# Performance work log

Hardware: AMD Instinct MI355X
Metric: run time of the kernel (lower is better)

Reference implementation:

```python
import jax, jax.numpy as jnp
import numpy as np

B, HH, WW = 4, 192, 192
DIM, HEADS, WIN, SHIFT, HID = 256, 8, 8, 4, 1024
EPS = 1e-5


def _rel_index(w):
    coords = np.stack(np.meshgrid(np.arange(w), np.arange(w), indexing='ij')).reshape(2, -1)
    rel = coords[:, :, None] - coords[:, None, :]            # [2, N, N]
    rel = rel.transpose(1, 2, 0).astype(np.int64)
    rel[:, :, 0] += w - 1
    rel[:, :, 1] += w - 1
    rel[:, :, 0] *= 2 * w - 1
    return rel.sum(-1)                                        # [N, N]


def _ln(x, g, b):
    m = x.mean(-1, keepdims=True)
    v = ((x - m) ** 2).mean(-1, keepdims=True)
    return (x - m) / jnp.sqrt(v + EPS) * g + b


def setup_inputs() -> dict:
    key = jax.random.key(0)
    ks = jax.random.split(key, 8)
    s = 0.02
    return {
        'x': jax.random.normal(ks[0], (B, HH * WW, DIM), jnp.float32),
        'norm1_g': jnp.ones((DIM,), jnp.float32),
        'norm1_b': jnp.zeros((DIM,), jnp.float32),
        'qkv_w': s * jax.random.normal(ks[1], (DIM, 3 * DIM), jnp.float32),
        'qkv_b': jnp.zeros((3 * DIM,), jnp.float32),
        'bias_table': s * jax.random.normal(ks[2], ((2 * WIN - 1) ** 2, HEADS), jnp.float32),
        'proj_w': s * jax.random.normal(ks[3], (DIM, DIM), jnp.float32),
        'proj_b': jnp.zeros((DIM,), jnp.float32),
        'norm2_g': jnp.ones((DIM,), jnp.float32),
        'norm2_b': jnp.zeros((DIM,), jnp.float32),
        'fc1_w': s * jax.random.normal(ks[4], (DIM, HID), jnp.float32),
        'fc1_b': jnp.zeros((HID,), jnp.float32),
        'fc2_w': s * jax.random.normal(ks[5], (HID, DIM), jnp.float32),
        'fc2_b': jnp.zeros((DIM,), jnp.float32),
        'H': HH,
        'W': WW,
    }


def reference(x, norm1_g, norm1_b, qkv_w, qkv_b, bias_table, proj_w, proj_b,
              norm2_g, norm2_b, fc1_w, fc1_b, fc2_w, fc2_b, H, W):
    Bn, L, C = x.shape
    hd = C // HEADS
    win = min(WIN, H, W)
    shift = SHIFT if win > SHIFT else 0
    shortcut = x

    h = _ln(x, norm1_g, norm1_b).reshape(Bn, H, W, C)
    pad_b = (win - H % win) % win
    pad_r = (win - W % win) % win
    h = jnp.pad(h, ((0, 0), (0, pad_b), (0, pad_r), (0, 0)))
    Hp, Wp = H + pad_b, W + pad_r
    if shift > 0:
        h = jnp.roll(h, (-shift, -shift), axis=(1, 2))

    nh, nw = Hp // win, Wp // win
    h = h.reshape(Bn, nh, win, nw, win, C).transpose(0, 1, 3, 2, 4, 5)
    h = h.reshape(Bn * nh * nw, win * win, C)
    N = win * win

    # windowed attention
    qkv = (h @ qkv_w + qkv_b).reshape(-1, N, 3, HEADS, hd)
    q, k, v = qkv[:, :, 0], qkv[:, :, 1], qkv[:, :, 2]      # [Bw, N, H, hd]
    scale = hd ** -0.5
    attn = jnp.einsum('bqhd,bkhd->bhqk', q * scale, k)
    rel_idx = jnp.asarray(_rel_index(win))                   # [N, N]
    bias = bias_table[rel_idx.reshape(-1)].reshape(N, N, HEADS).transpose(2, 0, 1)
    attn = jax.nn.softmax(attn + bias[None], axis=-1)
    o = jnp.einsum('bhqk,bkhd->bqhd', attn, v).reshape(-1, N, C)
    o = o @ proj_w + proj_b

    # window reverse
    o = o.reshape(Bn, nh, nw, win, win, C).transpose(0, 1, 3, 2, 4, 5).reshape(Bn, Hp, Wp, C)
    if shift > 0:
        o = jnp.roll(o, (shift, shift), axis=(1, 2))
    o = o[:, :H, :W, :].reshape(Bn, H * W, C)

    x = shortcut + o
    m = _ln(x, norm2_g, norm2_b)
    m = jax.nn.gelu(m @ fc1_w + fc1_b, approximate=False) @ fc2_w + fc2_b
    return x + m
```

## Files before the change

### kernel.cpp

```cpp
#include <hip/hip_runtime.h>


#define SHIFT_ 4

typedef __attribute__((ext_vector_type(8))) short short8;
typedef __attribute__((ext_vector_type(4))) float floatx4;

__device__ __forceinline__ unsigned short f2b(float f) {
  union { float f; unsigned int i; } c; c.f = f;
  unsigned int u = c.i;
  return (unsigned short)((u + 0x7FFFu + ((u >> 16) & 1u)) >> 16);
}

__device__ __forceinline__ float fast_gelu(float v) {
  const float u = v * v;
  const float z = v * (2.3022082f + 0.10294326f * u);
  const float e = __builtin_amdgcn_exp2f(z);
  const float r = __builtin_amdgcn_rcpf(1.f + e);
  return v - v * r;
}

__device__ __forceinline__ void load_lds16(const void* g, void* l) {
  __builtin_amdgcn_global_load_lds((__attribute__((address_space(1))) void*)g,
                                   (__attribute__((address_space(3))) void*)l, 16, 0, 0);
}

__device__ __forceinline__ size_t tok_of_row(int row) {
  int widx = row >> 6, t = row & 63;
  int b = widx / 576; int rem = widx - b * 576;
  int wy = rem / 24, wx = rem - wy * 24;
  int ti = t >> 3, tj = t & 7;
  int gr = wy * 8 + ti + SHIFT_; if (gr >= 192) gr -= 192;
  int gc = wx * 8 + tj + SHIFT_; if (gc >= 192) gc -= 192;
  return (size_t)b * 36864 + (size_t)(gr * 192 + gc);
}

template<int SHUFFLE>
__global__ __launch_bounds__(256) void ln_kernel(const float* __restrict__ src,
    const float* __restrict__ gw, const float* __restrict__ bw,
    unsigned short* __restrict__ dst) {
  const int lane = threadIdx.x & 63;
  const int m = blockIdx.x * 4 + (threadIdx.x >> 6);
  const size_t soff = SHUFFLE ? tok_of_row(m) * 256 : (size_t)m * 256;
  float4 xv = *(const float4*)(src + soff + lane * 4);
  float s  = xv.x + xv.y + xv.z + xv.w;
  float s2 = xv.x * xv.x + xv.y * xv.y + xv.z * xv.z + xv.w * xv.w;
  #pragma unroll
  for (int off = 32; off > 0; off >>= 1) { s += __shfl_xor(s, off); s2 += __shfl_xor(s2, off); }
  const float mean = s * 0.00390625f;
  const float var  = s2 * 0.00390625f - mean * mean;
  const float rstd = rsqrtf(var + 1e-5f);
  float4 gv = *(const float4*)(gw + lane * 4);
  float4 bv = *(const float4*)(bw + lane * 4);
  ushort4 o;
  o.x = f2b((xv.x - mean) * rstd * gv.x + bv.x);
  o.y = f2b((xv.y - mean) * rstd * gv.y + bv.y);
  o.z = f2b((xv.z - mean) * rstd * gv.z + bv.z);
  o.w = f2b((xv.w - mean) * rstd * gv.w + bv.w);
  *(ushort4*)(dst + (size_t)m * 256 + lane * 4) = o;
}

__global__ void wconv(const float* __restrict__ W, unsigned short* __restrict__ Wt,
                      int K, int N) {
  const int idx = blockIdx.x * 256 + threadIdx.x;
  const int n = idx / K, k = idx - n * K;
  Wt[idx] = f2b(W[(size_t)k * N + n]);
}

template<int MODE>
__global__ __launch_bounds__(256) void gemm_bt(
    const unsigned short* __restrict__ A, const unsigned short* __restrict__ Wt,
    const float* __restrict__ bias, const float* __restrict__ X,
    unsigned short* __restrict__ outb, float* __restrict__ outf,
    int Ntot, int K) {
  __shared__ unsigned short sm[16384];
  const int tid = threadIdx.x;
  const int wave = tid >> 6, lane = tid & 63;
  const int lr = lane & 15, lg = lane >> 4;
  const int wm = wave >> 1, wn = wave & 1;
  const int m0 = blockIdx.y * 128, n0 = blockIdx.x * 128;

  const unsigned short* rbase = (wave < 2) ? (A + (size_t)m0 * K)
                                           : (Wt + (size_t)n0 * K);
  unsigned short* ldsbase = &sm[wave * 4096];
  const int rc0 = (wave & 1) * 8;
  int off[8];
  #pragma unroll
  for (int t = 0; t < 8; ++t) {
    const int P = (rc0 + t) * 64 + lane;
    const int r = P >> 3, c = (P & 7) ^ (r & 7);
    off[t] = r * K + c * 8;
  }

  floatx4 acc[4][4];
  #pragma unroll
  for (int i = 0; i < 4; ++i)
    #pragma unroll
    for (int j = 0; j < 4; ++j) acc[i][j] = (floatx4)0.f;

  for (int k0 = 0; k0 < K; k0 += 64) {
    __syncthreads();
    #pragma unroll
    for (int t = 0; t < 8; ++t)
      load_lds16(rbase + (off[t] + k0), ldsbase + t * 512);
    __syncthreads();
    #pragma unroll
    for (int kk = 0; kk < 2; ++kk) {
      short8 af[4], bf[4];
      #pragma unroll
      for (int mi = 0; mi < 4; ++mi) {
        const int r = wm * 64 + mi * 16 + lr;
        af[mi] = *(const short8*)&sm[r * 64 + (((kk * 4 + lg) ^ (r & 7)) * 8)];
      }
      #pragma unroll
      for (int ni = 0; ni < 4; ++ni) {
        const int r = wn * 64 + ni * 16 + lr;
        bf[ni] = *(const short8*)&sm[8192 + r * 64 + (((kk * 4 + lg) ^ (r & 7)) * 8)];
      }
      #pragma unroll
      for (int mi = 0; mi < 4; ++mi)
        #pragma unroll
        for (int ni = 0; ni < 4; ++ni)
          acc[mi][ni] = __builtin_amdgcn_mfma_f32_16x16x32_bf16(af[mi], bf[ni], acc[mi][ni], 0, 0, 0);
    }
  }

  #pragma unroll
  for (int mi = 0; mi < 4; ++mi) {
    #pragma unroll
    for (int r = 0; r < 4; ++r) {
      const int row = m0 + wm * 64 + mi * 16 + lg * 4 + r;
      size_t obase;
      if (MODE == 1) obase = tok_of_row(row) * 256;
      else obase = (size_t)row * Ntot;
      #pragma unroll
      for (int ni = 0; ni < 4; ++ni) {
        const int col = n0 + wn * 64 + ni * 16 + lr;
        const float v = acc[mi][ni][r] + bias[col];
        if (MODE == 0) {
          outb[obase + col] = f2b(v);
        } else {
          outf[obase + col] = X[obase + col] + v;
        }
      }
    }
  }
}

__global__ __launch_bounds__(256, 2) void mlp_fused(
    float* xio, const float* __restrict__ gw, const float* __restrict__ bw,
    const unsigned short* __restrict__ w1, const float* __restrict__ b1,
    const unsigned short* __restrict__ w2, const float* __restrict__ b2) {
  __shared__ unsigned short smA[16384];
  __shared__ unsigned short smH[16384];
  const int tid = threadIdx.x;
  const int wave = tid >> 6, lane = tid & 63;
  const int lr = lane & 15, lg = lane >> 4;
  const int m0 = blockIdx.x * 64;

  {
    const float4 gv = *(const float4*)(gw + lane * 4);
    const float4 bv = *(const float4*)(bw + lane * 4);
    for (int rr = 0; rr < 16; ++rr) {
      const int row = wave * 16 + rr;
      float4 xv = *(const float4*)(xio + (size_t)(m0 + row) * 256 + lane * 4);
      float s  = xv.x + xv.y + xv.z + xv.w;
      float s2 = xv.x * xv.x + xv.y * xv.y + xv.z * xv.z + xv.w * xv.w;
      #pragma unroll
      for (int off = 32; off > 0; off >>= 1) { s += __shfl_xor(s, off); s2 += __shfl_xor(s2, off); }
      const float mean = s * 0.00390625f;
      const float var  = s2 * 0.00390625f - mean * mean;
      const float rstd = rsqrtf(var + 1e-5f);
      ushort4 o;
      o.x = f2b((xv.x - mean) * rstd * gv.x + bv.x);
      o.y = f2b((xv.y - mean) * rstd * gv.y + bv.y);
      o.z = f2b((xv.z - mean) * rstd * gv.z + bv.z);
      o.w = f2b((xv.w - mean) * rstd * gv.w + bv.w);
      const int idx = row * 256 + ((((lane >> 1) ^ (row & 7))) << 3) + (lane & 1) * 4;
      *(ushort4*)&smA[idx] = o;
    }
  }
  __syncthreads();

  float b2v[4];
  #pragma unroll
  for (int ni = 0; ni < 4; ++ni) b2v[ni] = b2[wave * 64 + ni * 16 + lr];

  floatx4 acc2[4][4];
  #pragma unroll
  for (int i = 0; i < 4; ++i)
    #pragma unroll
    for (int j = 0; j < 4; ++j) acc2[i][j] = (floatx4)0.f;

  for (int q = 0; q < 4; ++q) {
    floatx4 acc1[4][4];
    #pragma unroll
    for (int i = 0; i < 4; ++i)
      #pragma unroll
      for (int j = 0; j < 4; ++j) acc1[i][j] = (floatx4)0.f;

    const unsigned short* w1q = w1 + (size_t)(q * 256 + wave * 64) * 256;
    #pragma unroll
    for (int kk = 0; kk < 8; ++kk) {
      short8 af[4], bf[4];
      #pragma unroll
      for (int mi = 0; mi < 4; ++mi) {
        const int r = mi * 16 + lr;
        af[mi] = *(const short8*)&smA[r * 256 + (((kk * 4 + lg) ^ (r & 7)) << 3)];
      }
      #pragma unroll
      for (int ni = 0; ni < 4; ++ni)
        bf[ni] = *(const short8*)(w1q + (ni * 16 + lr) * 256 + kk * 32 + lg * 8);
      #pragma unroll
      for (int mi = 0; mi < 4; ++mi)
        #pragma unroll
        for (int ni = 0; ni < 4; ++ni)
          acc1[mi][ni] = __builtin_amdgcn_mfma_f32_16x16x32_bf16(af[mi], bf[ni], acc1[mi][ni], 0, 0, 0);
    }

    float b1v[4];
    #pragma unroll
    for (int ni = 0; ni < 4; ++ni) b1v[ni] = b1[q * 256 + wave * 64 + ni * 16 + lr];

    __syncthreads();
    #pragma unroll
    for (int mi = 0; mi < 4; ++mi)
      #pragma unroll
      for (int r = 0; r < 4; ++r) {
        const int row = mi * 16 + lg * 4 + r;
        const int rbase = row * 256, rx = row & 7;
        #pragma unroll
        for (int ni = 0; ni < 4; ++ni) {
          const int col = wave * 64 + ni * 16 + lr;
          const float v = acc1[mi][ni][r] + b1v[ni];
          smH[rbase + (((col >> 3) ^ rx) << 3) + (lr & 7)] = f2b(fast_gelu(v));
        }
      }
    __syncthreads();

    const unsigned short* w2q = w2 + q * 256;
    #pragma unroll
    for (int kk = 0; kk < 8; ++kk) {
      short8 af[4], bf[4];
      #pragma unroll
      for (int mi = 0; mi < 4; ++mi) {
        const int r = mi * 16 + lr;
        af[mi] = *(const short8*)&smH[r * 256 + (((kk * 4 + lg) ^ (r & 7)) << 3)];
      }
      #pragma unroll
      for (int ni = 0; ni < 4; ++ni)
        bf[ni] = *(const short8*)(w2q + (size_t)(wave * 64 + ni * 16 + lr) * 1024 + kk * 32 + lg * 8);
      #pragma unroll
      for (int mi = 0; mi < 4; ++mi)
        #pragma unroll
        for (int ni = 0; ni < 4; ++ni)
          acc2[mi][ni] = __builtin_amdgcn_mfma_f32_16x16x32_bf16(af[mi], bf[ni], acc2[mi][ni], 0, 0, 0);
    }
  }

  #pragma unroll
  for (int mi = 0; mi < 4; ++mi)
    #pragma unroll
    for (int r = 0; r < 4; ++r) {
      const size_t gbase = (size_t)(m0 + mi * 16 + lg * 4 + r) * 256;
      #pragma unroll
      for (int ni = 0; ni < 4; ++ni) {
        const int col = wave * 64 + ni * 16 + lr;
        xio[gbase + col] += acc2[mi][ni][r] + b2v[ni];
      }
    }
}

__global__ __launch_bounds__(64) void attn_kernel(const unsigned short* __restrict__ qkv,
    const float* __restrict__ btab, unsigned short* __restrict__ obuf) {
  __shared__ unsigned short vts[2048];
  __shared__ unsigned short ps[4096];
  __shared__ float bs[225];
  const int l = threadIdx.x;
  const int win = blockIdx.x >> 3, head = blockIdx.x & 7;
  const int lr = l & 15, lg = l >> 4;
  const unsigned short* base = qkv + (size_t)(win * 64) * 768 + head * 32;

  #pragma unroll
  for (int c = 0; c < 8; ++c) {
    ushort4 vv = *(const ushort4*)(base + (size_t)l * 768 + 512 + c * 4);
    #pragma unroll
    for (int j = 0; j < 4; ++j) {
      const int d = c * 4 + j;
      const unsigned short val = j == 0 ? vv.x : j == 1 ? vv.y : j == 2 ? vv.z : vv.w;
      vts[d * 64 + (((l >> 3) ^ (d & 7)) * 8) + (l & 7)] = val;
    }
  }
  for (int i = l; i < 225; i += 64) bs[i] = btab[i * 8 + head];

  short8 af[4], bfr[4];
  #pragma unroll
  for (int mi = 0; mi < 4; ++mi)
    af[mi] = *(const short8*)(base + (size_t)(mi * 16 + lr) * 768 + lg * 8);
  #pragma unroll
  for (int ni = 0; ni < 4; ++ni)
    bfr[ni] = *(const short8*)(base + (size_t)(ni * 16 + lr) * 768 + 256 + lg * 8);

  floatx4 sa[4][4];
  #pragma unroll
  for (int mi = 0; mi < 4; ++mi)
    #pragma unroll
    for (int ni = 0; ni < 4; ++ni)
      sa[mi][ni] = __builtin_amdgcn_mfma_f32_16x16x32_bf16(af[mi], bfr[ni], (floatx4)0.f, 0, 0, 0);

  __syncthreads();

  const float scale = 0.17677669529663687f;
  #pragma unroll
  for (int mi = 0; mi < 4; ++mi) {
    #pragma unroll
    for (int r = 0; r < 4; ++r) {
      const int qi = mi * 16 + lg * 4 + r;
      const int ti = qi >> 3, tj = qi & 7;
      float vals[4];
      #pragma unroll
      for (int ni = 0; ni < 4; ++ni) {
        const int kc = ni * 16 + lr;
        const int tk = kc >> 3, tl = kc & 7;
        vals[ni] = sa[mi][ni][r] * scale + bs[(ti - tk + 7) * 15 + (tj - tl + 7)];
      }
      float mx = fmaxf(fmaxf(vals[0], vals[1]), fmaxf(vals[2], vals[3]));
      #pragma unroll
      for (int off = 1; off < 16; off <<= 1) mx = fmaxf(mx, __shfl_xor(mx, off, 16));
      float se = 0.f;
      #pragma unroll
      for (int ni = 0; ni < 4; ++ni) { vals[ni] = __expf(vals[ni] - mx); se += vals[ni]; }
      #pragma unroll
      for (int off = 1; off < 16; off <<= 1) se += __shfl_xor(se, off, 16);
      const float inv = 1.f / se;
      #pragma unroll
      for (int ni = 0; ni < 4; ++ni) {
        const int col = ni * 16 + lr;
        const int cell = col >> 3;
        ps[qi * 64 + ((cell ^ (qi & 7)) * 8) + (col & 7)] = f2b(vals[ni] * inv);
      }
    }
  }
  __syncthreads();

  floatx4 oa[4][2];
  #pragma unroll
  for (int mi = 0; mi < 4; ++mi) { oa[mi][0] = (floatx4)0.f; oa[mi][1] = (floatx4)0.f; }
  #pragma unroll
  for (int kk = 0; kk < 2; ++kk) {
    short8 pa[4], vb[2];
    #pragma unroll
    for (int mi = 0; mi < 4; ++mi) {
      const int r = mi * 16 + lr;
      pa[mi] = *(const short8*)&ps[r * 64 + (((kk * 4 + lg) ^ (r & 7)) * 8)];
    }
    #pragma unroll
    for (int nj = 0; nj < 2; ++nj) {
      const int r = nj * 16 + lr;
      vb[nj] = *(const short8*)&vts[r * 64 + (((kk * 4 + lg) ^ (r & 7)) * 8)];
    }
    #pragma unroll
    for (int mi = 0; mi < 4; ++mi)
      #pragma unroll
      for (int nj = 0; nj < 2; ++nj)
        oa[mi][nj] = __builtin_amdgcn_mfma_f32_16x16x32_bf16(pa[mi], vb[nj], oa[mi][nj], 0, 0, 0);
  }
  #pragma unroll
  for (int mi = 0; mi < 4; ++mi)
    #pragma unroll
    for (int nj = 0; nj < 2; ++nj)
      #pragma unroll
      for (int r = 0; r < 4; ++r) {
        const int row = mi * 16 + lg * 4 + r, d = nj * 16 + lr;
        obuf[(size_t)(win * 64 + row) * 256 + head * 32 + d] = f2b(oa[mi][nj][r]);
      }
}

extern "C" void kernel_launch(void* const* d_in, const int* in_sizes, int n_in,
                              void* d_out, int out_size, void* d_ws, size_t ws_size,
                              hipStream_t stream) {
  (void)in_sizes; (void)n_in; (void)out_size; (void)ws_size;
  const float* x      = (const float*)d_in[0];
  const float* n1g    = (const float*)d_in[1];
  const float* n1b    = (const float*)d_in[2];
  const float* qkv_w  = (const float*)d_in[3];
  const float* qkv_b  = (const float*)d_in[4];
  const float* btab   = (const float*)d_in[5];
  const float* proj_w = (const float*)d_in[6];
  const float* proj_b = (const float*)d_in[7];
  const float* n2g    = (const float*)d_in[8];
  const float* n2b    = (const float*)d_in[9];
  const float* fc1_w  = (const float*)d_in[10];
  const float* fc1_b  = (const float*)d_in[11];
  const float* fc2_w  = (const float*)d_in[12];
  const float* fc2_b  = (const float*)d_in[13];
  float* out = (float*)d_out;

  char* wsb = (char*)d_ws;
  unsigned short* wqkv  = (unsigned short*)(wsb);
  unsigned short* wproj = (unsigned short*)(wsb + 393216);
  unsigned short* wfc1  = (unsigned short*)(wsb + 524288);
  unsigned short* wfc2  = (unsigned short*)(wsb + 1048576);
  unsigned short* hbuf  = (unsigned short*)(wsb + 1572864);
  unsigned short* big   = (unsigned short*)(wsb + 77070336);

  wconv<<<768, 256, 0, stream>>>(qkv_w, wqkv, 256, 768);
  wconv<<<256, 256, 0, stream>>>(proj_w, wproj, 256, 256);
  wconv<<<1024, 256, 0, stream>>>(fc1_w, wfc1, 256, 1024);
  wconv<<<1024, 256, 0, stream>>>(fc2_w, wfc2, 1024, 256);

  ln_kernel<1><<<36864, 256, 0, stream>>>(x, n1g, n1b, hbuf);
  gemm_bt<0><<<dim3(6, 1152), 256, 0, stream>>>(hbuf, wqkv, qkv_b, nullptr, big, nullptr, 768, 256);
  attn_kernel<<<18432, 64, 0, stream>>>(big, btab, hbuf);
  gemm_bt<1><<<dim3(2, 1152), 256, 0, stream>>>(hbuf, wproj, proj_b, x, nullptr, out, 256, 256);
  mlp_fused<<<2304, 256, 0, stream>>>(out, n2g, n2b, wfc1, fc1_b, wfc2, fc2_b);
}
```

Before: 978.5 us.

## Use 8 waves per block in fused MLP with transposed fc1 MFMA operands

The fused LN+MLP kernel now runs 512 threads (8 waves) per block instead of 4 waves. Each wave handles 32 hidden columns and 32 output columns, so the accumulator arrays shrink. The fc1 MFMA is transposed so weights are the A operand and tokens the B operand, which lets the GELU output be written to LDS as packed ushort4 with a 16-way XOR swizzle instead of scalar stores. The aim is more latency hiding, lower register pressure and fewer LDS store instructions. The cost is more waves competing for LDS and barriers, and more global weight reads per token tile.

```diff
diff --git a/kernel.cpp b/kernel.cpp
--- a/kernel.cpp
+++ b/kernel.cpp
@@ -147,7 +147,7 @@
   }
 }
 
-__global__ __launch_bounds__(256, 2) void mlp_fused(
+__global__ __launch_bounds__(512, 4) void mlp_fused(
     float* xio, const float* __restrict__ gw, const float* __restrict__ bw,
     const unsigned short* __restrict__ w1, const float* __restrict__ b1,
     const unsigned short* __restrict__ w2, const float* __restrict__ b2) {
@@ -161,8 +161,9 @@
   {
     const float4 gv = *(const float4*)(gw + lane * 4);
     const float4 bv = *(const float4*)(bw + lane * 4);
-    for (int rr = 0; rr < 16; ++rr) {
-      const int row = wave * 16 + rr;
+    #pragma unroll
+    for (int rr = 0; rr < 8; ++rr) {
+      const int row = wave * 8 + rr;
       float4 xv = *(const float4*)(xio + (size_t)(m0 + row) * 256 + lane * 4);
       float s  = xv.x + xv.y + xv.z + xv.w;
       float s2 = xv.x * xv.x + xv.y * xv.y + xv.z * xv.z + xv.w * xv.w;
@@ -176,85 +177,88 @@
       o.y = f2b((xv.y - mean) * rstd * gv.y + bv.y);
       o.z = f2b((xv.z - mean) * rstd * gv.z + bv.z);
       o.w = f2b((xv.w - mean) * rstd * gv.w + bv.w);
-      const int idx = row * 256 + ((((lane >> 1) ^ (row & 7))) << 3) + (lane & 1) * 4;
+      const int idx = row * 256 + ((((lane >> 1) ^ (row & 15))) << 3) + (lane & 1) * 4;
       *(ushort4*)&smA[idx] = o;
     }
   }
   __syncthreads();
 
-  float b2v[4];
-  #pragma unroll
-  for (int ni = 0; ni < 4; ++ni) b2v[ni] = b2[wave * 64 + ni * 16 + lr];
-
-  floatx4 acc2[4][4];
+  float b2v[2];
+  #pragma unroll
+  for (int nj = 0; nj < 2; ++nj) b2v[nj] = b2[wave * 32 + nj * 16 + lr];
+
+  floatx4 acc2[4][2];
   #pragma unroll
   for (int i = 0; i < 4; ++i)
     #pragma unroll
-    for (int j = 0; j < 4; ++j) acc2[i][j] = (floatx4)0.f;
+    for (int j = 0; j < 2; ++j) acc2[i][j] = (floatx4)0.f;
 
   for (int q = 0; q < 4; ++q) {
-    floatx4 acc1[4][4];
-    #pragma unroll
-    for (int i = 0; i < 4; ++i)
+    floatx4 acc1[2][4];
+    #pragma unroll
+    for (int i = 0; i < 2; ++i)
       #pragma unroll
       for (int j = 0; j < 4; ++j) acc1[i][j] = (floatx4)0.f;
 
-    const unsigned short* w1q = w1 + (size_t)(q * 256 + wave * 64) * 256;
+    const unsigned short* w1q = w1 + (size_t)(q * 256 + wave * 32) * 256;
     #pragma unroll
     for (int kk = 0; kk < 8; ++kk) {
-      short8 af[4], bf[4];
+      short8 af[2], bf[4];
+      #pragma unroll
+      for (int hi = 0; hi < 2; ++hi)
+        af[hi] = *(const short8*)(w1q + (hi * 16 + lr) * 256 + kk * 32 + lg * 8);
+      #pragma unroll
+      for (int ti = 0; ti < 4; ++ti) {
+        const int tok = ti * 16 + lr;
+        bf[ti] = *(const short8*)&smA[tok * 256 + (((kk * 4 + lg) ^ lr) << 3)];
+      }
+      #pragma unroll
+      for (int hi = 0; hi < 2; ++hi)
+        #pragma unroll
+        for (int ti = 0; ti < 4; ++ti)
+          acc1[hi][ti] = __builtin_amdgcn_mfma_f32_16x16x32_bf16(af[hi], bf[ti], acc1[hi][ti], 0, 0, 0);
+    }
+
+    float4 b1v[2];
+    #pragma unroll
+    for (int hi = 0; hi < 2; ++hi)
+      b1v[hi] = *(const float4*)(b1 + q * 256 + wave * 32 + hi * 16 + lg * 4);
+
+    __syncthreads();
+    #pragma unroll
+    for (int hi = 0; hi < 2; ++hi) {
+      const int cellbase = wave * 4 + hi * 2 + (lg >> 1);
+      #pragma unroll
+      for (int ti = 0; ti < 4; ++ti) {
+        const int tok = ti * 16 + lr;
+        ushort4 hv;
+        hv.x = f2b(fast_gelu(acc1[hi][ti][0] + b1v[hi].x));
+        hv.y = f2b(fast_gelu(acc1[hi][ti][1] + b1v[hi].y));
+        hv.z = f2b(fast_gelu(acc1[hi][ti][2] + b1v[hi].z));
+        hv.w = f2b(fast_gelu(acc1[hi][ti][3] + b1v[hi].w));
+        const int idx = tok * 256 + ((cellbase ^ lr) << 3) + (lg & 1) * 4;
+        *(ushort4*)&smH[idx] = hv;
+      }
+    }
+    __syncthreads();
+
+    const unsigned short* w2q = w2 + q * 256;
+    #pragma unroll
+    for (int kk = 0; kk < 8; ++kk) {
+      short8 af[4], bf[2];
       #pragma unroll
       for (int mi = 0; mi < 4; ++mi) {
-        const int r = mi * 16 + lr;
-        af[mi] = *(const short8*)&smA[r * 256 + (((kk * 4 + lg) ^ (r & 7)) << 3)];
-      }
-      #pragma unroll
-      for (int ni = 0; ni < 4; ++ni)
-        bf[ni] = *(const short8*)(w1q + (ni * 16 + lr) * 256 + kk * 32 + lg * 8);
+        const int tok = mi * 16 + lr;
+        af[mi] = *(const short8*)&smH[tok * 256 + (((kk * 4 + lg) ^ lr) << 3)];
+      }
+      #pragma unroll
+      for (int nj = 0; nj < 2; ++nj)
+        bf[nj] = *(const short8*)(w2q + (size_t)(wave * 32 + nj * 16 + lr) * 1024 + kk * 32 + lg * 8);
       #pragma unroll
       for (int mi = 0; mi < 4; ++mi)
         #pragma unroll
-        for (int ni = 0; ni < 4; ++ni)
-          acc1[mi][ni] = __builtin_amdgcn_mfma_f32_16x16x32_bf16(af[mi], bf[ni], acc1[mi][ni], 0, 0, 0);
-    }
-
-    float b1v[4];
-    #pragma unroll
-    for (int ni = 0; ni < 4; ++ni) b1v[ni] = b1[q * 256 + wave * 64 + ni * 16 + lr];
-
-    __syncthreads();
-    #pragma unroll
-    for (int mi = 0; mi < 4; ++mi)
-      #pragma unroll
-      for (int r = 0; r < 4; ++r) {
-        const int row = mi * 16 + lg * 4 + r;
-        const int rbase = row * 256, rx = row & 7;
-        #pragma unroll
-        for (int ni = 0; ni < 4; ++ni) {
-          const int col = wave * 64 + ni * 16 + lr;
-          const float v = acc1[mi][ni][r] + b1v[ni];
-          smH[rbase + (((col >> 3) ^ rx) << 3) + (lr & 7)] = f2b(fast_gelu(v));
-        }
-      }
-    __syncthreads();
-
-    const unsigned short* w2q = w2 + q * 256;
-    #pragma unroll
-    for (int kk = 0; kk < 8; ++kk) {
-      short8 af[4], bf[4];
-      #pragma unroll
-      for (int mi = 0; mi < 4; ++mi) {
-        const int r = mi * 16 + lr;
-        af[mi] = *(const short8*)&smH[r * 256 + (((kk * 4 + lg) ^ (r & 7)) << 3)];
-      }
-      #pragma unroll
-      for (int ni = 0; ni < 4; ++ni)
-        bf[ni] = *(const short8*)(w2q + (size_t)(wave * 64 + ni * 16 + lr) * 1024 + kk * 32 + lg * 8);
-      #pragma unroll
-      for (int mi = 0; mi < 4; ++mi)
-        #pragma unroll
-        for (int ni = 0; ni < 4; ++ni)
-          acc2[mi][ni] = __builtin_amdgcn_mfma_f32_16x16x32_bf16(af[mi], bf[ni], acc2[mi][ni], 0, 0, 0);
+        for (int nj = 0; nj < 2; ++nj)
+          acc2[mi][nj] = __builtin_amdgcn_mfma_f32_16x16x32_bf16(af[mi], bf[nj], acc2[mi][nj], 0, 0, 0);
     }
   }
 
@@ -264,9 +268,9 @@
     for (int r = 0; r < 4; ++r) {
       const size_t gbase = (size_t)(m0 + mi * 16 + lg * 4 + r) * 256;
       #pragma unroll
-      for (int ni = 0; ni < 4; ++ni) {
-        const int col = wave * 64 + ni * 16 + lr;
-        xio[gbase + col] += acc2[mi][ni][r] + b2v[ni];
+      for (int nj = 0; nj < 2; ++nj) {
+        const int col = wave * 32 + nj * 16 + lr;
+        xio[gbase + col] += acc2[mi][nj][r] + b2v[nj];
       }
     }
 }
@@ -413,5 +417,5 @@
   gemm_bt<0><<<dim3(6, 1152), 256, 0, stream>>>(hbuf, wqkv, qkv_b, nullptr, big, nullptr, 768, 256);
   attn_kernel<<<18432, 64, 0, stream>>>(big, btab, hbuf);
   gemm_bt<1><<<dim3(2, 1152), 256, 0, stream>>>(hbuf, wproj, proj_b, x, nullptr, out, 256, 256);
-  mlp_fused<<<2304, 256, 0, stream>>>(out, n2g, n2b, wfc1, fc1_b, wfc2, fc2_b);
-}
+  mlp_fused<<<2304, 512, 0, stream>>>(out, n2g, n2b, wfc1, fc1_b, wfc2, fc2_b);
+}
```

Result: faster. 911.1 us (-6.9%).
